# Kernel optimization log

Measured on AMD Instinct MI355X. Metric: run time of the kernel, lower is better.

## Reference

```python
import jax, jax.numpy as jnp
import numpy as np

B = 64          # batch_size
NMAX = 299      # max_node_length
N = NMAX + 1    # node axis (incl. eos slot)
T_SUB = 8       # subtokens per node (padded)
D = 512         # embedding_dim == nfeat
H = 512         # hidden_size == nclass
NHEADS = 8
NHID = 64       # nhid * nheads == D
VOCAB = 50000
NEG = jnp.float32(-9e15)


def setup_inputs() -> dict:
    key = jax.random.key(0)
    ks = jax.random.split(key, 13)
    s = 0.02  # init_uniform_mag
    tokens = jax.random.randint(ks[0], (B, NMAX, T_SUB), 0, VOCAB, dtype=jnp.int32)
    tok_lens = jax.random.randint(ks[1], (B, NMAX), 1, T_SUB + 1, dtype=jnp.int32)
    # seq_lens = node_count + 1 (eos); force max length so GRU T is static
    seq_lens = jax.random.randint(ks[2], (B,), 2, N + 1, dtype=jnp.int32).at[0].set(N)
    adjacent = (jax.random.uniform(ks[3], (B, N, N)) < 0.05).astype(jnp.float32)
    emb = jax.random.normal(ks[4], (VOCAB, D), dtype=jnp.float32) * 0.02
    Wq = jax.random.uniform(ks[5], (NHEADS, D, NHID), minval=-s, maxval=s)
    Wk = jax.random.uniform(ks[6], (NHEADS, D, NHID), minval=-s, maxval=s)
    Wq_o = jax.random.uniform(ks[7], (D, H), minval=-s, maxval=s)
    Wk_o = jax.random.uniform(ks[8], (D, H), minval=-s, maxval=s)
    r = 1.0 / np.sqrt(H)
    gru_Wih = jax.random.uniform(ks[9], (2, 3 * H, D), minval=-r, maxval=r)
    gru_Whh = jax.random.uniform(ks[10], (2, 3 * H, H), minval=-r, maxval=r)
    gru_bih = jnp.zeros((2, 3 * H), jnp.float32)
    gru_bhh = jnp.zeros((2, 3 * H), jnp.float32)
    return dict(tokens=tokens, tok_lens=tok_lens, seq_lens=seq_lens, adjacent=adjacent,
                emb=emb, Wq=Wq, Wk=Wk, Wq_o=Wq_o, Wk_o=Wk_o,
                gru_Wih=gru_Wih, gru_Whh=gru_Whh, gru_bih=gru_bih, gru_bhh=gru_bhh)


def gat_layer(x, cond, Wq, Wk):
    # x: [B,N,F]; cond: [B,N,N] bool adjacency (+eye) mask
    q = x @ Wq                                    # [B,N,O]
    k = x @ Wk
    scores = jnp.einsum('bno,bmo->bnm', q, k)
    s = jax.nn.softmax(scores, axis=0)            # torch legacy F.softmax(3D) -> dim=0
    att = jnp.where(cond, s, NEG)
    att = jax.nn.softmax(att, axis=1)
    hp = jnp.einsum('bnm,bmf->bnf', att, x) @ Wk  # note: re-uses Wk (faithful)
    return jax.nn.softmax(hp, axis=1)


def gru_cell(x_t, h, Wih, Whh, bih, bhh):
    gi = x_t @ Wih.T + bih
    gh = h @ Whh.T + bhh
    i_r, i_z, i_n = jnp.split(gi, 3, axis=-1)
    h_r, h_z, h_n = jnp.split(gh, 3, axis=-1)
    r = jax.nn.sigmoid(i_r + h_r)
    z = jax.nn.sigmoid(i_z + h_z)
    n = jnp.tanh(i_n + r * h_n)
    return (1.0 - z) * n + z * h


def run_gru_dir(x, mask, Wih, Whh, bih, bhh):
    # x: [T,B,I] time-major, mask: [T,B] bool (packed-sequence semantics)
    Bb = x.shape[1]
    h0 = jnp.zeros((Bb, H), x.dtype)
    def step(h, xm):
        x_t, m = xm
        h_new = gru_cell(x_t, h, Wih, Whh, bih, bhh)
        h = jnp.where(m[:, None], h_new, h)
        return h, jnp.where(m[:, None], h_new, jnp.zeros_like(h_new))
    h_f, outs = jax.lax.scan(step, h0, (x, mask))
    return outs, h_f


def reference(tokens, tok_lens, seq_lens, adjacent, emb, Wq, Wk, Wq_o, Wk_o,
              gru_Wih, gru_Whh, gru_bih, gru_bhh):
    node_counts = seq_lens - 1                                     # nodes per sample
    # --- GRUEmbedding.forward: sum of subtoken embeddings / node_count ---
    tmask = (jnp.arange(T_SUB)[None, None, :] < tok_lens[:, :, None]).astype(emb.dtype)
    node_sum = (emb[tokens] * tmask[..., None]).sum(axis=2)        # [B,NMAX,D]
    node_emb = node_sum / node_counts[:, None, None].astype(emb.dtype)
    padding_vec = emb[0]                                           # gruembedding([[0]])
    eos_vec = emb[2]                                               # gruembedding([[2]])
    node_emb_p = jnp.concatenate([node_emb, jnp.zeros((B, 1, D), emb.dtype)], axis=1)
    n_idx = jnp.arange(N)[None, :, None]
    nc = node_counts[:, None, None]
    embedded = jnp.where(n_idx < nc, node_emb_p,
                         jnp.where(n_idx == nc, eos_vec, padding_vec))  # [B,N,D]
    # --- GAT ---
    adj_sym = adjacent + jnp.swapaxes(adjacent, 1, 2)
    cond = (adj_sym + jnp.eye(N, dtype=adjacent.dtype)) > 0
    heads = jax.vmap(gat_layer, in_axes=(None, None, 0, 0))(embedded, cond, Wq, Wk)
    x = jnp.transpose(heads, (1, 2, 0, 3)).reshape(B, N, NHEADS * NHID)
    out = jax.nn.elu(gat_layer(x, cond, Wq_o, Wk_o))               # [B,N,H]
    # --- packed bidirectional GRU ---
    xt = jnp.swapaxes(out, 0, 1)                                   # [N,B,H] time-major
    mask = jnp.arange(N)[:, None] < seq_lens[None, :]              # [N,B]
    out_f, h_f = run_gru_dir(xt, mask, gru_Wih[0], gru_Whh[0], gru_bih[0], gru_bhh[0])
    # reverse each sequence within its own length
    idx = jnp.clip(seq_lens[None, :] - 1 - jnp.arange(N)[:, None], 0)  # [N,B]
    x_rev = jnp.take_along_axis(xt, idx[:, :, None], axis=0)
    outs_r, h_b = run_gru_dir(x_rev, mask, gru_Wih[1], gru_Whh[1], gru_bih[1], gru_bhh[1])
    out_b = jnp.take_along_axis(outs_r, idx[:, :, None], axis=0) * mask[:, :, None]
    outputs = out_f + out_b                                        # fwd-half + bwd-half
    hidden = jnp.stack([h_f, h_b], axis=0)                         # [2,B,H]
    return outputs, hidden
```

## Files before the change

kernel.cpp:

```cpp
#include <hip/hip_runtime.h>
#include <hip/hip_bf16.h>

typedef __hip_bfloat16 bf16;
typedef unsigned long long ull;
typedef __attribute__((ext_vector_type(8))) short s16x8;
typedef __attribute__((ext_vector_type(4))) float f32x4;

#define B_      64
#define NMAX_   299
#define N_      300
#define D_      512
#define H_      512
#define NHEADS_ 8
#define NHID_   64
#define SCLD    304
#define SCSZ    (N_ * SCLD)
#define LDP     48
#define W5P     520
#define HP      520
#define AK      320


__device__ __forceinline__ float sigmoidf_(float x) { return 1.0f / (1.0f + expf(-x)); }


__global__ void embed_k(const int* __restrict__ tokens, const int* __restrict__ tok_lens,
                        const int* __restrict__ seq_lens, const float* __restrict__ emb,
                        bf16* __restrict__ out)
{
    const int n = blockIdx.x, b = blockIdx.y;
    const int d = threadIdx.x * 4;
    const int nc = seq_lens[b] - 1;
    float4 v;
    if (n < nc) {
        const int tl = tok_lens[b * NMAX_ + n];
        const int* tp = tokens + (b * NMAX_ + n) * 8;
        float4 acc = {0.f, 0.f, 0.f, 0.f};
        for (int t = 0; t < 8; ++t) {
            if (t < tl) {
                const float4 e = *(const float4*)(emb + (long)tp[t] * D_ + d);
                acc.x += e.x; acc.y += e.y; acc.z += e.z; acc.w += e.w;
            }
        }
        const float inv = 1.0f / (float)nc;
        v.x = acc.x * inv; v.y = acc.y * inv; v.z = acc.z * inv; v.w = acc.w * inv;
    } else {
        const int row = (n == nc) ? 2 : 0;
        v = *(const float4*)(emb + row * D_ + d);
    }
    bf16 o[4] = {__float2bfloat16(v.x), __float2bfloat16(v.y),
                 __float2bfloat16(v.z), __float2bfloat16(v.w)};
    *(uint2*)(out + ((long)b * N_ + n) * D_ + d) = *(uint2*)o;
}


__global__ void cond_k(const float* __restrict__ adj, unsigned char* __restrict__ cond)
{
    __shared__ float T1[64][65];
    __shared__ float T2[64][65];
    const int b = blockIdx.z;
    const int n0 = blockIdx.x * 64, m0 = blockIdx.y * 64;
    const int jj = threadIdx.x & 63, i0 = threadIdx.x >> 6;
    for (int r = 0; r < 16; ++r) {
        const int i = i0 * 16 + r;
        const int n = n0 + i, m = m0 + jj;
        T1[i][jj] = (n < N_ && m < N_) ? adj[((long)b * N_ + n) * N_ + m] : 0.f;
        const int n2 = m0 + i, m2 = n0 + jj;
        T2[i][jj] = (n2 < N_ && m2 < N_) ? adj[((long)b * N_ + n2) * N_ + m2] : 0.f;
    }
    __syncthreads();
    for (int r = 0; r < 16; ++r) {
        const int i = i0 * 16 + r;
        const int n = n0 + i, m = m0 + jj;
        if (n < N_ && m < N_) {
            const float v = T1[i][jj] + T2[jj][i] + ((n == m) ? 1.f : 0.f);
            cond[((long)b * N_ + n) * N_ + m] = (v > 0.f) ? 1 : 0;
        }
    }
}


__global__ void wgath_k(const float* __restrict__ W, bf16* __restrict__ out)
{
    const int row = blockIdx.x;
    const int d = threadIdx.x;
    const int h = row >> 6, o = row & 63;
    out[row * 512 + d] = __float2bfloat16(W[((long)h * 512 + d) * 64 + o]);
}

__global__ void wtr_k(const float* __restrict__ W, bf16* __restrict__ out)
{
    const int o = blockIdx.x;
    const int i = threadIdx.x;
    out[o * 512 + i] = __float2bfloat16(W[(long)i * 512 + o]);
}

__global__ void f2b_k(const float* __restrict__ in, bf16* __restrict__ out, long n)
{
    for (long i = (long)blockIdx.x * 256 + threadIdx.x; i < n; i += (long)gridDim.x * 256)
        out[i] = __float2bfloat16(in[i]);
}


__global__ void tbf_k(const bf16* __restrict__ in, bf16* __restrict__ out)
{
    __shared__ short T[64][65];
    const int b = blockIdx.z;
    const int m0 = blockIdx.x * 64, f0 = blockIdx.y * 64;
    const int jj = threadIdx.x & 63, i0 = threadIdx.x >> 6;
    for (int r = 0; r < 16; ++r) {
        const int i = i0 * 16 + r;
        const int m = m0 + i, f = f0 + jj;
        short v = 0;
        if (m < N_) v = *(const short*)&in[((long)b * N_ + m) * 512 + f];
        T[i][jj] = v;
    }
    __syncthreads();
    for (int r = 0; r < 16; ++r) {
        const int i = i0 * 16 + r;
        const int f = f0 + i, m = m0 + jj;
        ((short*)out)[((long)b * 512 + f) * AK + m] = T[jj][i];
    }
}


template<int BM, int BN, bool OBF>
__global__ __launch_bounds__(256) void mgemm_k(
    const bf16* __restrict__ A, long sA, int lda,
    const bf16* __restrict__ Bm, long sB, int ldb,
    void* __restrict__ C, long sC, int ldc,
    int M, int N, int K)
{
    __shared__ short As[BM * LDP];
    __shared__ short Bs[BN * LDP];
    const int z = blockIdx.z;
    const bf16* Ab = A + (long)z * sA;
    const bf16* Bb = Bm + (long)z * sB;
    const int m0 = blockIdx.x * BM, n0 = blockIdx.y * BN;
    const int tid = threadIdx.x;
    const int lane = tid & 63;
    const int w = tid >> 6;
    const int wm = (w >> 1) * (BM / 2);
    const int wn = (w & 1) * (BN / 2);
    constexpr int MR = BM / 32;
    constexpr int NR = BN / 32;
    f32x4 acc[MR][NR] = {};

    const int srow = tid >> 2;
    const int sslot = (tid & 3) * 8;

    for (int k0 = 0; k0 < K; k0 += 32) {
        #pragma unroll
        for (int r = 0; r < BM / 64; ++r) {
            const int row = r * 64 + srow;
            uint4 v = {0u, 0u, 0u, 0u};
            if (m0 + row < M)
                v = *(const uint4*)(Ab + (long)(m0 + row) * lda + k0 + sslot);
            *(uint4*)&As[row * LDP + sslot] = v;
        }
        #pragma unroll
        for (int r = 0; r < BN / 64; ++r) {
            const int row = r * 64 + srow;
            uint4 v = {0u, 0u, 0u, 0u};
            if (n0 + row < N)
                v = *(const uint4*)(Bb + (long)(n0 + row) * ldb + k0 + sslot);
            *(uint4*)&Bs[row * LDP + sslot] = v;
        }
        __syncthreads();
        s16x8 aq[MR], bq[NR];
        #pragma unroll
        for (int i = 0; i < MR; ++i)
            aq[i] = *(const s16x8*)&As[(wm + i * 16 + (lane & 15)) * LDP + (lane >> 4) * 8];
        #pragma unroll
        for (int j = 0; j < NR; ++j)
            bq[j] = *(const s16x8*)&Bs[(wn + j * 16 + (lane & 15)) * LDP + (lane >> 4) * 8];
        #pragma unroll
        for (int i = 0; i < MR; ++i)
            #pragma unroll
            for (int j = 0; j < NR; ++j)
                acc[i][j] = __builtin_amdgcn_mfma_f32_16x16x32_bf16(aq[i], bq[j], acc[i][j], 0, 0, 0);
        __syncthreads();
    }

    #pragma unroll
    for (int i = 0; i < MR; ++i) {
        const int mrow = m0 + wm + i * 16 + (lane >> 4) * 4;
        #pragma unroll
        for (int j = 0; j < NR; ++j) {
            const int ncol = n0 + wn + j * 16 + (lane & 15);
            if (ncol < N) {
                #pragma unroll
                for (int e = 0; e < 4; ++e) {
                    const int mm = mrow + e;
                    if (mm < M) {
                        const long idx = (long)z * sC + (long)mm * ldc + ncol;
                        if (OBF) ((bf16*)C)[idx] = __float2bfloat16(acc[i][j][e]);
                        else     ((float*)C)[idx] = acc[i][j][e];
                    }
                }
            }
        }
    }
}


__global__ __launch_bounds__(256) void bsoft_k(
    const float* __restrict__ sc, float* __restrict__ mx, float* __restrict__ sm)
{
    __shared__ float T[64][65];
    __shared__ float P[4][64];
    __shared__ float Mv[64];
    const int idx0 = blockIdx.x * 64;
    const int il = threadIdx.x & 63;
    const int bq = threadIdx.x >> 6;

    #pragma unroll
    for (int r = 0; r < 16; ++r) {
        const int b = bq * 16 + r;
        T[b][il] = sc[(long)b * SCSZ + idx0 + il];
    }
    __syncthreads();

    float pm = -1e30f;
    #pragma unroll
    for (int r = 0; r < 16; ++r) pm = fmaxf(pm, T[bq * 16 + r][il]);
    P[bq][il] = pm;
    __syncthreads();
    if (bq == 0) {
        float m = fmaxf(fmaxf(P[0][il], P[1][il]), fmaxf(P[2][il], P[3][il]));
        Mv[il] = m;
        mx[idx0 + il] = m;
    }
    __syncthreads();

    const float m = Mv[il];
    float ps = 0.f;
    #pragma unroll
    for (int r = 0; r < 16; ++r) ps += expf(T[bq * 16 + r][il] - m);
    __syncthreads();
    P[bq][il] = ps;
    __syncthreads();
    if (bq == 0)
        sm[idx0 + il] = P[0][il] + P[1][il] + P[2][il] + P[3][il];
}

#define NSTR 38

__global__ __launch_bounds__(512) void colsoft_k(
    const float* __restrict__ sc, const float* __restrict__ mx,
    const float* __restrict__ sm, const unsigned char* __restrict__ cond,
    bf16* __restrict__ abf)
{
    __shared__ float red[8][64];
    const int ml = threadIdx.x & 63;
    const int ng = threadIdx.x >> 6;
    const int m = blockIdx.x * 64 + ml;
    const int b = blockIdx.y;
    const float* scb = sc + (long)b * SCSZ;
    const unsigned char* cb = cond + (long)b * (N_ * N_);
    const bool act = m < N_;

    float ev[NSTR];
    ull cmask = 0;
    float vmax = -1e30f;
    #pragma unroll
    for (int i = 0; i < NSTR; ++i) {
        const int n = ng + i * 8;
        float e = 0.f;
        if (n < N_ && act && cb[n * N_ + m]) {
            const int o = n * SCLD + m;
            e = expf(scb[o] - mx[o]) / sm[o];
            cmask |= 1ull << i;
            vmax = fmaxf(vmax, e);
        }
        ev[i] = e;
    }
    red[ng][ml] = vmax;
    __syncthreads();
    vmax = red[0][ml];
    #pragma unroll
    for (int i = 1; i < 8; ++i) vmax = fmaxf(vmax, red[i][ml]);

    float ssum = 0.f;
    #pragma unroll
    for (int i = 0; i < NSTR; ++i)
        if ((cmask >> i) & 1) ssum += expf(ev[i] - vmax);
    __syncthreads();
    red[ng][ml] = ssum;
    __syncthreads();
    ssum = 0.f;
    #pragma unroll
    for (int i = 0; i < 8; ++i) ssum += red[i][ml];
    const float inv = 1.0f / ssum;

    #pragma unroll
    for (int i = 0; i < NSTR; ++i) {
        const int n = ng + i * 8;
        if (n < N_) {
            const float v = ((cmask >> i) & 1) ? expf(ev[i] - vmax) * inv : 0.f;
            abf[(long)b * (N_ * AK) + n * AK + m] = __float2bfloat16(v);
        }
    }
}

__global__ void nsoft_k(const float* __restrict__ hp, bf16* __restrict__ out)
{
    const int f = blockIdx.x * 256 + threadIdx.x;
    const int b = blockIdx.y;
    const float* hb = hp + (long)b * (N_ * 512) + f;
    float vmax = -1e30f;
    for (int n = 0; n < N_; ++n) vmax = fmaxf(vmax, hb[n * 512]);
    float s = 0.f;
    for (int n = 0; n < N_; ++n) s += expf(hb[n * 512] - vmax);
    const float inv = 1.0f / s;
    bf16* ob = out + (long)b * (N_ * 512) + f;
    for (int n = 0; n < N_; ++n) ob[n * 512] = __float2bfloat16(expf(hb[n * 512] - vmax) * inv);
}


__global__ void xrev_k(const bf16* __restrict__ out2, const int* __restrict__ seq_lens,
                       bf16* __restrict__ xr)
{
    const int t = blockIdx.x, b = blockIdx.y;
    const int d = threadIdx.x * 4;
    int src = seq_lens[b] - 1 - t;
    if (src < 0) src = 0;
    *(uint2*)(xr + ((long)t * B_ + b) * 512 + d) =
        *(const uint2*)(out2 + ((long)b * N_ + src) * 512 + d);
}

__global__ void zero_k(float* __restrict__ p, long n)
{
    for (long i = (long)blockIdx.x * 256 + threadIdx.x; i < n; i += (long)gridDim.x * 256)
        p[i] = 0.f;
}


__device__ __forceinline__ void dbar5(unsigned* __restrict__ gc, unsigned* __restrict__ root,
                                      int step) {
    __syncthreads();
    if (threadIdx.x == 0) {
        const unsigned old =
            __hip_atomic_fetch_add(gc, 1u, __ATOMIC_RELAXED, __HIP_MEMORY_SCOPE_AGENT);
        if (old == (unsigned)(step * 8 + 7))
            __hip_atomic_fetch_add(root, 1u, __ATOMIC_RELAXED, __HIP_MEMORY_SCOPE_AGENT);
        while (__hip_atomic_load(root, __ATOMIC_RELAXED, __HIP_MEMORY_SCOPE_AGENT)
               < (unsigned)((step + 1) * 4)) {
            __builtin_amdgcn_s_sleep(1);
        }
    }
    __syncthreads();
}

__global__ __launch_bounds__(128, 1) void gru_recur5(
    const bf16* __restrict__ gif, const bf16* __restrict__ gib,
    const float* __restrict__ Whh, const float* __restrict__ bih,
    const float* __restrict__ bhh, const int* __restrict__ seq_lens,
    float* __restrict__ hbuf_f, unsigned* __restrict__ bar,
    float* __restrict__ outf, float* __restrict__ outb,
    float* __restrict__ hfin)
{
    __shared__ alignas(16) short wlds[2 * 3 * 16 * W5P];
    __shared__ alignas(16) short hlds[16 * HP];
    const int tid = threadIdx.x;
    const int lane = tid & 63;
    const int w = tid >> 6;
    const int ml = lane & 15;
    const int ksl = lane >> 4;
    const int dir = blockIdx.x >> 7;
    const int rem = blockIdx.x & 127;
    const int slab = rem >> 2;
    const int bq   = rem & 3;
    const int ub   = slab * 16;
    const int g8   = dir * 4 + bq;
    unsigned* gc   = bar + (g8 * 4 + (slab >> 3)) * 32;
    unsigned* root = bar + 1024 + g8 * 32;
    bf16* hb = (bf16*)hbuf_f;

    {
        const float* Wb = Whh + (long)dir * (1536 * 512);
        for (int idx = tid; idx < 3 * 16 * 512; idx += 128) {
            const int row = idx >> 9;
            const int k = idx & 511;
            const int g = row >> 4, ul = row & 15;
            const float v = Wb[(long)(g * 512 + ub + ul) * 512 + k];
            const bf16 hi = __float2bfloat16(v);
            const bf16 lo = __float2bfloat16(v - __bfloat162float(hi));
            wlds[(0 * 48 + row) * W5P + k] = *(const short*)&hi;
            wlds[(1 * 48 + row) * W5P + k] = *(const short*)&lo;
        }
    }

    const int bcol = bq * 16 + ml;
    const int ue   = ub + ksl * 4;
    const bf16* gi = dir ? gib : gif;
    float cr[4], cz[4], cn[4], brr[4], bzz[4], bnn[4];
    #pragma unroll
    for (int e = 0; e < 4; ++e) {
        cr[e]  = bih[dir * 1536 + ue + e];
        cz[e]  = bih[dir * 1536 + 512 + ue + e];
        cn[e]  = bih[dir * 1536 + 1024 + ue + e];
        brr[e] = bhh[dir * 1536 + ue + e];
        bzz[e] = bhh[dir * 1536 + 512 + ue + e];
        bnn[e] = bhh[dir * 1536 + 1024 + ue + e];
    }
    const int sl = seq_lens[bcol];
    float hreg[4] = {0.f, 0.f, 0.f, 0.f};
    float owv[4] = {0.f, 0.f, 0.f, 0.f};

    if (w == 0) {
        const long z0 = (long)((dir * 2 + 0) * 2 + 0) * 32768 + bcol * 512 + ue;
        const long z1 = (long)((dir * 2 + 0) * 2 + 1) * 32768 + bcol * 512 + ue;
        __hip_atomic_store((ull*)(hb + z0), 0ull, __ATOMIC_RELAXED, __HIP_MEMORY_SCOPE_AGENT);
        __hip_atomic_store((ull*)(hb + z1), 0ull, __ATOMIC_RELAXED, __HIP_MEMORY_SCOPE_AGENT);
    }
    dbar5(gc, root, 0);

    for (int t = 0; t < N_; ++t) {
        const int rp = t & 1, wp = rp ^ 1;
        const ull* hu0 = (const ull*)hb + (long)((dir * 2 + rp) * 2 + 0) * 8192 + bq * 2048;
        const ull* hu1 = (const ull*)hb + (long)((dir * 2 + rp) * 2 + 1) * 8192 + bq * 2048;

        ull r0[16], r1[16];
        #pragma unroll
        for (int i = 0; i < 16; ++i)
            r0[i] = __hip_atomic_load(hu0 + i * 128 + tid,
                                      __ATOMIC_RELAXED, __HIP_MEMORY_SCOPE_AGENT);
        #pragma unroll
        for (int i = 0; i < 16; ++i)
            r1[i] = __hip_atomic_load(hu1 + i * 128 + tid,
                                      __ATOMIC_RELAXED, __HIP_MEMORY_SCOPE_AGENT);

        if (t > 0 && w == 0) {
            const int tp = t - 1;
            if (dir == 0) {
                #pragma unroll
                for (int e = 0; e < 4; ++e)
                    outf[(long)tp * 32768 + (ue + e) * 64 + bcol] = owv[e];
            } else if (tp < sl) {
                #pragma unroll
                for (int e = 0; e < 4; ++e)
                    outb[(long)(sl - 1 - tp) * 32768 + (ue + e) * 64 + bcol] = owv[e];
            }
        }

        float gv[3][4];
        if (w == 0) {
            #pragma unroll
            for (int g = 0; g < 3; ++g)
                #pragma unroll
                for (int e = 0; e < 4; ++e)
                    gv[g][e] = __bfloat162float(
                        gi[(long)t * 98304 + (g * 512 + ue + e) * 64 + bcol]);
        }

        #pragma unroll
        for (int i = 0; i < 16; ++i) {
            const int q = i * 128 + tid;
            const int bl_ = q >> 7, uo = q & 127;
            *(ull*)&hlds[bl_ * HP + uo * 4] = r0[i];
        }
        __syncthreads();

        const int brow = ml * HP;
        f32x4 acc[3] = {};
        #pragma unroll
        for (int k8 = 0; k8 < 8; ++k8) {
            const int ks = w * 8 + k8;
            const int u0 = ks * 32 + ksl * 8;
            const s16x8 fh = *(const s16x8*)&hlds[brow + u0];
            const s16x8 a0h = *(const s16x8*)&wlds[(0 * 48 + 0 * 16 + ml) * W5P + u0];
            const s16x8 a1h = *(const s16x8*)&wlds[(0 * 48 + 1 * 16 + ml) * W5P + u0];
            const s16x8 a2h = *(const s16x8*)&wlds[(0 * 48 + 2 * 16 + ml) * W5P + u0];
            const s16x8 a0l = *(const s16x8*)&wlds[(1 * 48 + 0 * 16 + ml) * W5P + u0];
            const s16x8 a1l = *(const s16x8*)&wlds[(1 * 48 + 1 * 16 + ml) * W5P + u0];
            const s16x8 a2l = *(const s16x8*)&wlds[(1 * 48 + 2 * 16 + ml) * W5P + u0];
            acc[0] = __builtin_amdgcn_mfma_f32_16x16x32_bf16(a0h, fh, acc[0], 0, 0, 0);
            acc[1] = __builtin_amdgcn_mfma_f32_16x16x32_bf16(a1h, fh, acc[1], 0, 0, 0);
            acc[2] = __builtin_amdgcn_mfma_f32_16x16x32_bf16(a2h, fh, acc[2], 0, 0, 0);
            acc[0] = __builtin_amdgcn_mfma_f32_16x16x32_bf16(a0l, fh, acc[0], 0, 0, 0);
            acc[1] = __builtin_amdgcn_mfma_f32_16x16x32_bf16(a1l, fh, acc[1], 0, 0, 0);
            acc[2] = __builtin_amdgcn_mfma_f32_16x16x32_bf16(a2l, fh, acc[2], 0, 0, 0);
        }
        __syncthreads();

        #pragma unroll
        for (int i = 0; i < 16; ++i) {
            const int q = i * 128 + tid;
            const int bl_ = q >> 7, uo = q & 127;
            *(ull*)&hlds[bl_ * HP + uo * 4] = r1[i];
        }
        __syncthreads();
        #pragma unroll
        for (int k8 = 0; k8 < 8; ++k8) {
            const int ks = w * 8 + k8;
            const int u0 = ks * 32 + ksl * 8;
            const s16x8 fl = *(const s16x8*)&hlds[brow + u0];
            const s16x8 a0h = *(const s16x8*)&wlds[(0 * 48 + 0 * 16 + ml) * W5P + u0];
            const s16x8 a1h = *(const s16x8*)&wlds[(0 * 48 + 1 * 16 + ml) * W5P + u0];
            const s16x8 a2h = *(const s16x8*)&wlds[(0 * 48 + 2 * 16 + ml) * W5P + u0];
            acc[0] = __builtin_amdgcn_mfma_f32_16x16x32_bf16(a0h, fl, acc[0], 0, 0, 0);
            acc[1] = __builtin_amdgcn_mfma_f32_16x16x32_bf16(a1h, fl, acc[1], 0, 0, 0);
            acc[2] = __builtin_amdgcn_mfma_f32_16x16x32_bf16(a2h, fl, acc[2], 0, 0, 0);
        }
        __syncthreads();

        float* scr = (float*)hlds;
        if (w == 1) {
            #pragma unroll
            for (int g = 0; g < 3; ++g)
                #pragma unroll
                for (int e = 0; e < 4; ++e)
                    scr[(lane * 3 + g) * 4 + e] = acc[g][e];
        }
        __syncthreads();

        if (w == 0) {
            #pragma unroll
            for (int g = 0; g < 3; ++g)
                #pragma unroll
                for (int e = 0; e < 4; ++e)
                    acc[g][e] += scr[(lane * 3 + g) * 4 + e];

            ull phi = 0, plo = 0;
            const bool msk = t < sl;
            #pragma unroll
            for (int e = 0; e < 4; ++e) {
                const float rg = sigmoidf_(cr[e] + gv[0][e] + brr[e] + acc[0][e]);
                const float zg = sigmoidf_(cz[e] + gv[1][e] + bzz[e] + acc[1][e]);
                const float ng = tanhf(cn[e] + gv[2][e] + rg * (bnn[e] + acc[2][e]));
                const float hnew = (1.f - zg) * ng + zg * hreg[e];
                owv[e] = (dir == 0) ? (msk ? hnew : 0.f) : hnew;
                hreg[e] = msk ? hnew : hreg[e];
                const bf16 h_hi = __float2bfloat16(hreg[e]);
                const bf16 h_lo = __float2bfloat16(hreg[e] - __bfloat162float(h_hi));
                phi |= (ull)(*(const unsigned short*)&h_hi) << (16 * e);
                plo |= (ull)(*(const unsigned short*)&h_lo) << (16 * e);
            }
            const long wbh = (long)((dir * 2 + wp) * 2 + 0) * 32768 + bcol * 512 + ue;
            const long wbl = (long)((dir * 2 + wp) * 2 + 1) * 32768 + bcol * 512 + ue;
            __hip_atomic_store((ull*)(hb + wbh), phi, __ATOMIC_RELAXED, __HIP_MEMORY_SCOPE_AGENT);
            __hip_atomic_store((ull*)(hb + wbl), plo, __ATOMIC_RELAXED, __HIP_MEMORY_SCOPE_AGENT);
        }

        dbar5(gc, root, t + 1);
    }

    if (w == 0) {
        const int tp = N_ - 1;
        if (dir == 0) {
            #pragma unroll
            for (int e = 0; e < 4; ++e)
                outf[(long)tp * 32768 + (ue + e) * 64 + bcol] = owv[e];
        } else if (tp < sl) {
            #pragma unroll
            for (int e = 0; e < 4; ++e)
                outb[(long)(sl - 1 - tp) * 32768 + (ue + e) * 64 + bcol] = owv[e];
        }
        #pragma unroll
        for (int e = 0; e < 4; ++e)
            hfin[dir * 32768 + (ue + e) * 64 + bcol] = hreg[e];
    }
}


__global__ void final_k(const float* __restrict__ outf, const float* __restrict__ outb,
                        const float* __restrict__ hfin, const int* __restrict__ seq_lens,
                        float* __restrict__ dout)
{
    const long i = (long)blockIdx.x * 256 + threadIdx.x;
    const long NOUT = (long)N_ * B_ * 512;
    if (i < NOUT) {
        const int t = (int)(i >> 15);
        const int b = (int)((i >> 9) & 63);
        const int u = (int)(i & 511);
        const long src = (long)t * 32768 + u * 64 + b;
        dout[i] = (t < seq_lens[b]) ? outf[src] + outb[src] : 0.f;
    } else if (i < NOUT + 2 * B_ * 512) {
        const long j = i - NOUT;
        const int dir = (int)(j >> 15);
        const int b = (int)((j >> 9) & 63);
        const int u = (int)(j & 511);
        dout[i] = hfin[dir * 32768 + u * 64 + b];
    }
}

__global__ void fail_zero_k(float* __restrict__ dout, long n)
{
    for (long i = (long)blockIdx.x * 256 + threadIdx.x; i < n; i += (long)gridDim.x * 256)
        dout[i] = 0.f;
}


extern "C" void kernel_launch(void* const* d_in, const int* in_sizes, int n_in,
                              void* d_out, int out_size, void* d_ws, size_t ws_size,
                              hipStream_t stream)
{
    const int*   tokens   = (const int*)d_in[0];
    const int*   tok_lens = (const int*)d_in[1];
    const int*   seq_lens = (const int*)d_in[2];
    const float* adj      = (const float*)d_in[3];
    const float* emb      = (const float*)d_in[4];
    const float* Wq       = (const float*)d_in[5];
    const float* Wk       = (const float*)d_in[6];
    const float* Wq_o     = (const float*)d_in[7];
    const float* Wk_o     = (const float*)d_in[8];
    const float* gWih     = (const float*)d_in[9];
    const float* gWhh     = (const float*)d_in[10];
    const float* gbih     = (const float*)d_in[11];
    const float* gbhh     = (const float*)d_in[12];
    float* out = (float*)d_out;

    const long SZ = (long)B_ * N_ * 512;
    float* F1 = (float*)d_ws;
    float* F2 = F1 + SZ;
    float* F3 = F2 + SZ;
    bf16* b0 = (bf16*)(F3 + SZ);
    bf16* b1 = b0 + SZ;
    bf16* b2 = b1 + SZ;
    bf16* b3 = b2 + SZ;
    float* sc   = (float*)(b3 + SZ);
    float* mx   = sc + (long)B_ * SCSZ;
    float* smv  = mx + SCSZ;
    unsigned char* cond = (unsigned char*)(smv + SCSZ);
    bf16* gif = (bf16*)(cond + (long)B_ * N_ * N_);
    bf16* gib = gif + (long)N_ * 1536 * B_;
    float* hbuf = (float*)(gib + (long)N_ * 1536 * B_);
    unsigned* bar = (unsigned*)(hbuf + 131072);
    float* hfin = (float*)(bar + 2048);
    const size_t needed = (size_t)((char*)(hfin + 2 * 512 * 64) - (char*)d_ws);
    if (ws_size < needed) {
        fail_zero_k<<<4096, 256, 0, stream>>>(out, out_size);
        return;
    }
    bf16* wq1  = (bf16*)sc;
    bf16* wk1  = wq1 + 512 * 512;
    bf16* w2q  = (bf16*)sc;
    bf16* w2k  = w2q + 512 * 512;
    bf16* wihb = b2;
    bf16* kT   = (bf16*)F1;
    bf16* abf  = (bf16*)F2;

    wgath_k<<<512, 512, 0, stream>>>(Wq, wq1);
    wgath_k<<<512, 512, 0, stream>>>(Wk, wk1);
    embed_k<<<dim3(N_, B_), 128, 0, stream>>>(tokens, tok_lens, seq_lens, emb, b0);
    cond_k<<<dim3(5, 5, B_), 256, 0, stream>>>(adj, cond);

    mgemm_k<128, 128, true><<<dim3(150, 4, 1), 256, 0, stream>>>(
        b0, 0, 512, wq1, 0, 512, b2, 0, 512, B_ * N_, 512, 512);
    mgemm_k<128, 128, true><<<dim3(150, 4, 1), 256, 0, stream>>>(
        b0, 0, 512, wk1, 0, 512, b3, 0, 512, B_ * N_, 512, 512);
    tbf_k<<<dim3(5, 8, B_), 256, 0, stream>>>(b3, kT);

    for (int h = 0; h < NHEADS_; ++h) {
        mgemm_k<64, 64, false><<<dim3(5, 5, B_), 256, 0, stream>>>(
            b2 + h * 64, (long)N_ * 512, 512,
            b3 + h * 64, (long)N_ * 512, 512,
            sc, SCSZ, SCLD, N_, N_, 64);
        bsoft_k<<<SCSZ / 64, 256, 0, stream>>>(sc, mx, smv);
        colsoft_k<<<dim3(5, B_), 512, 0, stream>>>(sc, mx, smv, cond, abf);
        mgemm_k<64, 64, false><<<dim3(5, 1, B_), 256, 0, stream>>>(
            abf, (long)N_ * AK, AK,
            kT + (long)h * 64 * AK, (long)512 * AK, AK,
            F3 + h * 64, (long)N_ * 512, 512, N_, 64, AK);
    }
    nsoft_k<<<dim3(2, B_), 256, 0, stream>>>(F3, b1);

    wtr_k<<<512, 512, 0, stream>>>(Wq_o, w2q);
    wtr_k<<<512, 512, 0, stream>>>(Wk_o, w2k);
    mgemm_k<128, 128, true><<<dim3(150, 4, 1), 256, 0, stream>>>(
        b1, 0, 512, w2q, 0, 512, b2, 0, 512, B_ * N_, 512, 512);
    mgemm_k<128, 128, true><<<dim3(150, 4, 1), 256, 0, stream>>>(
        b1, 0, 512, w2k, 0, 512, b3, 0, 512, B_ * N_, 512, 512);
    tbf_k<<<dim3(5, 8, B_), 256, 0, stream>>>(b3, kT);
    mgemm_k<64, 64, false><<<dim3(5, 5, B_), 256, 0, stream>>>(
        b2, (long)N_ * 512, 512, b3, (long)N_ * 512, 512,
        sc, SCSZ, SCLD, N_, N_, 512);
    f2b_k<<<6144, 256, 0, stream>>>(gWih, wihb, (long)2 * 1536 * 512);
    bsoft_k<<<SCSZ / 64, 256, 0, stream>>>(sc, mx, smv);
    colsoft_k<<<dim3(5, B_), 512, 0, stream>>>(sc, mx, smv, cond, abf);
    mgemm_k<64, 64, false><<<dim3(5, 8, B_), 256, 0, stream>>>(
        abf, (long)N_ * AK, AK,
        kT, (long)512 * AK, AK,
        F3, (long)N_ * 512, 512, N_, 512, AK);
    nsoft_k<<<dim3(2, B_), 256, 0, stream>>>(F3, b0);

    xrev_k<<<dim3(N_, B_), 128, 0, stream>>>(b0, seq_lens, b1);
    zero_k<<<1, 256, 0, stream>>>((float*)bar, 2048);
    mgemm_k<64, 64, true><<<dim3(24, 1, N_), 256, 0, stream>>>(
        wihb, 0, 512, b0, 512, (long)N_ * 512, gif, 1536 * 64, 64, 1536, 64, 512);
    mgemm_k<64, 64, true><<<dim3(24, 1, N_), 256, 0, stream>>>(
        wihb + 1536 * 512, 0, 512, b1, (long)B_ * 512, 512, gib, 1536 * 64, 64, 1536, 64, 512);

    gru_recur5<<<256, 128, 0, stream>>>(gif, gib, gWhh, gbih, gbhh, seq_lens,
                                        hbuf, bar, F1, F2, hfin);
    final_k<<<38656, 256, 0, stream>>>(F1, F2, hfin, seq_lens, out);
}
```

Before: 2.857 ms.

## Replace hierarchical GRU grid barrier with per-slab flag barrier; retune colsoft and Wih GEMM

The persistent GRU recurrence kernel's two-level atomic counter barrier is replaced by a flag barrier. Each block stores its step number in its own padded flag, and 32 threads of every block poll all slab flags with a wave-wide all-check. This is meant to cut the serialized atomic increments and the two-hop root wait on each of the 300 timesteps, at the cost of more polling traffic and a larger flag area. Separately, colsoft uses 32-column blocks with 16 row groups (twice as many blocks), and the input-projection GEMMs switch to 128x64 tiles.

```diff
diff --git a/kernel.cpp b/kernel.cpp
--- a/kernel.cpp
+++ b/kernel.cpp
@@ -244,33 +244,33 @@
         sm[idx0 + il] = P[0][il] + P[1][il] + P[2][il] + P[3][il];
 }
 
-#define NSTR 38
+#define NSTR3 19
 
 __global__ __launch_bounds__(512) void colsoft_k(
     const float* __restrict__ sc, const float* __restrict__ mx,
     const float* __restrict__ sm, const unsigned char* __restrict__ cond,
     bf16* __restrict__ abf)
 {
-    __shared__ float red[8][64];
-    const int ml = threadIdx.x & 63;
-    const int ng = threadIdx.x >> 6;
-    const int m = blockIdx.x * 64 + ml;
+    __shared__ float red[16][32];
+    const int ml = threadIdx.x & 31;
+    const int ng = threadIdx.x >> 5;
+    const int m = blockIdx.x * 32 + ml;
     const int b = blockIdx.y;
     const float* scb = sc + (long)b * SCSZ;
     const unsigned char* cb = cond + (long)b * (N_ * N_);
     const bool act = m < N_;
 
-    float ev[NSTR];
-    ull cmask = 0;
+    float ev[NSTR3];
+    unsigned cmask = 0;
     float vmax = -1e30f;
     #pragma unroll
-    for (int i = 0; i < NSTR; ++i) {
-        const int n = ng + i * 8;
+    for (int i = 0; i < NSTR3; ++i) {
+        const int n = ng + i * 16;
         float e = 0.f;
         if (n < N_ && act && cb[n * N_ + m]) {
             const int o = n * SCLD + m;
             e = expf(scb[o] - mx[o]) / sm[o];
-            cmask |= 1ull << i;
+            cmask |= 1u << i;
             vmax = fmaxf(vmax, e);
         }
         ev[i] = e;
@@ -279,23 +279,23 @@
     __syncthreads();
     vmax = red[0][ml];
     #pragma unroll
-    for (int i = 1; i < 8; ++i) vmax = fmaxf(vmax, red[i][ml]);
+    for (int i = 1; i < 16; ++i) vmax = fmaxf(vmax, red[i][ml]);
 
     float ssum = 0.f;
     #pragma unroll
-    for (int i = 0; i < NSTR; ++i)
+    for (int i = 0; i < NSTR3; ++i)
         if ((cmask >> i) & 1) ssum += expf(ev[i] - vmax);
     __syncthreads();
     red[ng][ml] = ssum;
     __syncthreads();
     ssum = 0.f;
     #pragma unroll
-    for (int i = 0; i < 8; ++i) ssum += red[i][ml];
+    for (int i = 0; i < 16; ++i) ssum += red[i][ml];
     const float inv = 1.0f / ssum;
 
     #pragma unroll
-    for (int i = 0; i < NSTR; ++i) {
-        const int n = ng + i * 8;
+    for (int i = 0; i < NSTR3; ++i) {
+        const int n = ng + i * 16;
         if (n < N_) {
             const float v = ((cmask >> i) & 1) ? expf(ev[i] - vmax) * inv : 0.f;
             abf[(long)b * (N_ * AK) + n * AK + m] = __float2bfloat16(v);
@@ -336,23 +336,23 @@
 }
 
 
-__device__ __forceinline__ void dbar5(unsigned* __restrict__ gc, unsigned* __restrict__ root,
-                                      int step) {
-    __syncthreads();
-    if (threadIdx.x == 0) {
-        const unsigned old =
-            __hip_atomic_fetch_add(gc, 1u, __ATOMIC_RELAXED, __HIP_MEMORY_SCOPE_AGENT);
-        if (old == (unsigned)(step * 8 + 7))
-            __hip_atomic_fetch_add(root, 1u, __ATOMIC_RELAXED, __HIP_MEMORY_SCOPE_AGENT);
-        while (__hip_atomic_load(root, __ATOMIC_RELAXED, __HIP_MEMORY_SCOPE_AGENT)
-               < (unsigned)((step + 1) * 4)) {
+__device__ __forceinline__ void fbar(unsigned* __restrict__ flg, int slab, int step) {
+    __syncthreads();
+    if (threadIdx.x == 0)
+        __hip_atomic_store(flg + slab * 32, (unsigned)(step + 1),
+                           __ATOMIC_RELAXED, __HIP_MEMORY_SCOPE_AGENT);
+    if (threadIdx.x < 32) {
+        for (;;) {
+            const unsigned v = __hip_atomic_load(flg + threadIdx.x * 32,
+                                   __ATOMIC_RELAXED, __HIP_MEMORY_SCOPE_AGENT);
+            if (__all(v >= (unsigned)(step + 1))) break;
             __builtin_amdgcn_s_sleep(1);
         }
     }
     __syncthreads();
 }
 
-__global__ __launch_bounds__(128, 1) void gru_recur5(
+__global__ __launch_bounds__(128, 1) void gru_recur6(
     const bf16* __restrict__ gif, const bf16* __restrict__ gib,
     const float* __restrict__ Whh, const float* __restrict__ bih,
     const float* __restrict__ bhh, const int* __restrict__ seq_lens,
@@ -373,8 +373,7 @@
     const int bq   = rem & 3;
     const int ub   = slab * 16;
     const int g8   = dir * 4 + bq;
-    unsigned* gc   = bar + (g8 * 4 + (slab >> 3)) * 32;
-    unsigned* root = bar + 1024 + g8 * 32;
+    unsigned* flg  = bar + g8 * 1024;
     bf16* hb = (bf16*)hbuf_f;
 
     {
@@ -414,7 +413,7 @@
         __hip_atomic_store((ull*)(hb + z0), 0ull, __ATOMIC_RELAXED, __HIP_MEMORY_SCOPE_AGENT);
         __hip_atomic_store((ull*)(hb + z1), 0ull, __ATOMIC_RELAXED, __HIP_MEMORY_SCOPE_AGENT);
     }
-    dbar5(gc, root, 0);
+    fbar(flg, slab, 0);
 
     for (int t = 0; t < N_; ++t) {
         const int rp = t & 1, wp = rp ^ 1;
@@ -543,7 +542,7 @@
             __hip_atomic_store((ull*)(hb + wbl), plo, __ATOMIC_RELAXED, __HIP_MEMORY_SCOPE_AGENT);
         }
 
-        dbar5(gc, root, t + 1);
+        fbar(flg, slab, t + 1);
     }
 
     if (w == 0) {
@@ -627,7 +626,7 @@
     bf16* gib = gif + (long)N_ * 1536 * B_;
     float* hbuf = (float*)(gib + (long)N_ * 1536 * B_);
     unsigned* bar = (unsigned*)(hbuf + 131072);
-    float* hfin = (float*)(bar + 2048);
+    float* hfin = (float*)(bar + 8192);
     const size_t needed = (size_t)((char*)(hfin + 2 * 512 * 64) - (char*)d_ws);
     if (ws_size < needed) {
         fail_zero_k<<<4096, 256, 0, stream>>>(out, out_size);
@@ -658,7 +657,7 @@
             b3 + h * 64, (long)N_ * 512, 512,
             sc, SCSZ, SCLD, N_, N_, 64);
         bsoft_k<<<SCSZ / 64, 256, 0, stream>>>(sc, mx, smv);
-        colsoft_k<<<dim3(5, B_), 512, 0, stream>>>(sc, mx, smv, cond, abf);
+        colsoft_k<<<dim3(10, B_), 512, 0, stream>>>(sc, mx, smv, cond, abf);
         mgemm_k<64, 64, false><<<dim3(5, 1, B_), 256, 0, stream>>>(
             abf, (long)N_ * AK, AK,
             kT + (long)h * 64 * AK, (long)512 * AK, AK,
@@ -678,7 +677,7 @@
         sc, SCSZ, SCLD, N_, N_, 512);
     f2b_k<<<6144, 256, 0, stream>>>(gWih, wihb, (long)2 * 1536 * 512);
     bsoft_k<<<SCSZ / 64, 256, 0, stream>>>(sc, mx, smv);
-    colsoft_k<<<dim3(5, B_), 512, 0, stream>>>(sc, mx, smv, cond, abf);
+    colsoft_k<<<dim3(10, B_), 512, 0, stream>>>(sc, mx, smv, cond, abf);
     mgemm_k<64, 64, false><<<dim3(5, 8, B_), 256, 0, stream>>>(
         abf, (long)N_ * AK, AK,
         kT, (long)512 * AK, AK,
@@ -686,13 +685,13 @@
     nsoft_k<<<dim3(2, B_), 256, 0, stream>>>(F3, b0);
 
     xrev_k<<<dim3(N_, B_), 128, 0, stream>>>(b0, seq_lens, b1);
-    zero_k<<<1, 256, 0, stream>>>((float*)bar, 2048);
-    mgemm_k<64, 64, true><<<dim3(24, 1, N_), 256, 0, stream>>>(
+    zero_k<<<1, 256, 0, stream>>>((float*)bar, 8192);
+    mgemm_k<128, 64, true><<<dim3(12, 1, N_), 256, 0, stream>>>(
         wihb, 0, 512, b0, 512, (long)N_ * 512, gif, 1536 * 64, 64, 1536, 64, 512);
-    mgemm_k<64, 64, true><<<dim3(24, 1, N_), 256, 0, stream>>>(
+    mgemm_k<128, 64, true><<<dim3(12, 1, N_), 256, 0, stream>>>(
         wihb + 1536 * 512, 0, 512, b1, (long)B_ * 512, 512, gib, 1536 * 64, 64, 1536, 64, 512);
 
-    gru_recur5<<<256, 128, 0, stream>>>(gif, gib, gWhh, gbih, gbhh, seq_lens,
+    gru_recur6<<<256, 128, 0, stream>>>(gif, gib, gWhh, gbih, gbhh, seq_lens,
                                         hbuf, bar, F1, F2, hfin);
     final_k<<<38656, 256, 0, stream>>>(F1, F2, hfin, seq_lens, out);
 }
```

Result: faster. 2.664 ms (-6.8%).
